# Performance work log

Measured on AMD Instinct MI355X. Metric: run time of the kernel, lower is better.

The kernel has to match this reference:

```python
import jax, jax.numpy as jnp
import numpy as np

B, N, D = 2, 2048, 1024
H = 16
HS = D // H
EPS = 1e-6


def layer_norm(x, scale, bias):
    mu = jnp.mean(x, axis=-1, keepdims=True)
    var = jnp.mean(jnp.square(x - mu), axis=-1, keepdims=True)
    return (x - mu) * jax.lax.rsqrt(var + EPS) * scale + bias


def setup_inputs() -> dict:
    key = jax.random.key(0)
    ks = jax.random.split(key, 8)
    lecun = lambda k, shape: jax.random.normal(k, shape, jnp.float32) / jnp.sqrt(shape[0])
    return {
        "x": jax.random.normal(ks[0], (B, N, D), jnp.float32),
        "ln1_scale": jnp.ones((D,), jnp.float32),
        "ln1_bias": jnp.zeros((D,), jnp.float32),
        "w_qkv": lecun(ks[1], (D, 3 * D)),
        "w_out": lecun(ks[2], (D, D)),
        "b_out": jnp.zeros((D,), jnp.float32),
        "ln2_scale": jnp.ones((D,), jnp.float32),
        "ln2_bias": jnp.zeros((D,), jnp.float32),
        "w1": lecun(ks[3], (D, 2 * D)),
        "b1": jnp.zeros((2 * D,), jnp.float32),
        "w2": lecun(ks[4], (2 * D, D)),
        "b2": jnp.zeros((D,), jnp.float32),
    }


def reference(x, ln1_scale, ln1_bias, w_qkv, w_out, b_out,
              ln2_scale, ln2_bias, w1, b1, w2, b2):
    b, n, d = x.shape
    # --- attention sub-block ---
    xn = layer_norm(x, ln1_scale, ln1_bias)
    qkv = xn @ w_qkv                      # [B,N,3D]
    q, k, v = jnp.split(qkv, 3, axis=-1)
    q = q.reshape(b, n, H, HS)
    k = k.reshape(b, n, H, HS)
    v = v.reshape(b, n, H, HS)
    scores = jnp.einsum('bihd,bjhd->bhij', q, k) / jnp.sqrt(jnp.float32(HS))
    causal = jnp.tril(jnp.ones((n, n), bool))[None, None]
    scores = jnp.where(causal, scores, -jnp.inf)
    attn = jax.nn.softmax(scores, axis=-1)
    out_heads = jnp.einsum('bhij,bjhd->bihd', attn, v).reshape(b, n, d)
    x = x + out_heads @ w_out + b_out
    xn2 = layer_norm(x, ln2_scale, ln2_bias)
    y = jax.nn.gelu(xn2 @ w1 + b1)        # flax nn.gelu default approximate=True
    x = x + (y @ w2 + b2)
    return x
```

## Files before the change

### kernel.cpp

```cpp
#include <hip/hip_runtime.h>

#define D_MODEL 1024
#define NSEQ    2048
#define NBATCH  2
#define NHEAD   16
#define HSZ     64
#define MROWS   4096

typedef short s8v  __attribute__((ext_vector_type(8)));
typedef float f32x4 __attribute__((ext_vector_type(4)));
typedef float f32x16 __attribute__((ext_vector_type(16)));
typedef unsigned long long u64;

#define AS1(p) ((__attribute__((address_space(1))) const void*)(p))
#define AS3(p) ((__attribute__((address_space(3))) void*)(p))

__device__ __forceinline__ float b2f(unsigned short s) {
    union { unsigned u; float f; } z; z.u = (unsigned)s << 16; return z.f;
}
__device__ __forceinline__ unsigned short f2b(float f) {
    union { float f; unsigned u; } z; z.f = f;
    unsigned r = z.u + 0x7fffu + ((z.u >> 16) & 1u);
    return (unsigned short)(r >> 16);
}
__device__ __forceinline__ float gelu_f(float x) {
    float u = 0.7978845608028654f * (x + 0.044715f * x * x * x);
    float t = 1.f - 2.f / (1.f + __expf(2.f * u));
    return 0.5f * x * (1.f + t);
}
__device__ __forceinline__ unsigned cvt_pk_bf16(float lo, float hi) {
    unsigned r;
    asm("v_cvt_pk_bf16_f32 %0, %1, %2" : "=v"(r) : "v"(lo), "v"(hi));
    return r;
}

__global__ __launch_bounds__(256) void sniff_k(const unsigned short* __restrict__ xr,
                                               int* __restrict__ flag) {
    __shared__ int cnt[4];
    int tid = threadIdx.x, ok = 0;
    for (int i = tid; i < 2048; i += 256) {
        unsigned short u = xr[i];
        int e = (u >> 7) & 0xFF;
        if (u == 0 || (e >= 110 && e <= 135)) ok++;
    }
    #pragma unroll
    for (int off = 32; off; off >>= 1) ok += __shfl_down(ok, off);
    if ((tid & 63) == 0) cnt[tid >> 6] = ok;
    __syncthreads();
    if (tid == 0) {
        int tot = cnt[0] + cnt[1] + cnt[2] + cnt[3];
        *flag = (tot > 1843) ? 1 : 0;
    }
}

__global__ __launch_bounds__(256) void cvt_small_k(
    const void* p0, const void* p1, const void* p2, const void* p3,
    const void* p4, const void* p5, const void* p6,
    unsigned short* __restrict__ out, const int* __restrict__ flag)
{
    int i = blockIdx.x * 256 + threadIdx.x;
    const void* src; int off;
    if      (i < 1024) { src = p0; off = i; }
    else if (i < 2048) { src = p1; off = i - 1024; }
    else if (i < 3072) { src = p2; off = i - 2048; }
    else if (i < 4096) { src = p3; off = i - 3072; }
    else if (i < 5120) { src = p4; off = i - 4096; }
    else if (i < 7168) { src = p5; off = i - 5120; }
    else               { src = p6; off = i - 7168; }
    out[i] = (*flag) ? ((const unsigned short*)src)[off]
                     : f2b(((const float*)src)[off]);
}

__global__ __launch_bounds__(256) void transpose_all_k(
    const void* wqkv, const void* wout, const void* w1, const void* w2,
    unsigned short* t_qkv, unsigned short* t_out,
    unsigned short* t_w1, unsigned short* t_w2, const int* __restrict__ flag)
{
    __shared__ unsigned short t[32][33];
    int bid = blockIdx.x;
    const void* W; unsigned short* Wt; int K, N, bx, by;
    if      (bid < 3072) { W = wqkv; Wt = t_qkv; K = 1024; N = 3072; bx = bid % 96; by = bid / 96; }
    else if (bid < 4096) { bid -= 3072; W = wout; Wt = t_out; K = 1024; N = 1024; bx = bid % 32; by = bid / 32; }
    else if (bid < 6144) { bid -= 4096; W = w1;   Wt = t_w1;  K = 1024; N = 2048; bx = bid % 64; by = bid / 64; }
    else                 { bid -= 6144; W = w2;   Wt = t_w2;  K = 2048; N = 1024; bx = bid % 32; by = bid / 32; }
    int f = *flag;
    int n0 = bx * 32, k0 = by * 32;
    int x = threadIdx.x & 31, y = threadIdx.x >> 5;
    #pragma unroll
    for (int r = 0; r < 32; r += 8) {
        size_t idx = (size_t)(k0 + r + y) * N + n0 + x;
        t[r + y][x] = f ? ((const unsigned short*)W)[idx]
                        : f2b(((const float*)W)[idx]);
    }
    __syncthreads();
    #pragma unroll
    for (int r = 0; r < 32; r += 8)
        Wt[(size_t)(n0 + r + y) * K + k0 + x] = t[x][r + y];
}

__global__ __launch_bounds__(256) void ln1f_k(
    const void* __restrict__ x_raw, const unsigned short* __restrict__ scale,
    const unsigned short* __restrict__ bias, unsigned short* __restrict__ xb,
    unsigned short* __restrict__ xn, const int* __restrict__ flag)
{
    int row = blockIdx.x, tid = threadIdx.x;
    int f = *flag;
    float v[4], s = 0.f, s2 = 0.f;
    #pragma unroll
    for (int i = 0; i < 4; ++i) {
        size_t idx = (size_t)row * D_MODEL + tid + i * 256;
        float t = f ? b2f(((const unsigned short*)x_raw)[idx])
                    : ((const float*)x_raw)[idx];
        v[i] = t; s += t; s2 += t * t;
    }
    #pragma unroll
    for (int off = 32; off; off >>= 1) { s += __shfl_down(s, off); s2 += __shfl_down(s2, off); }
    __shared__ float rs[4], rs2[4];
    int w = tid >> 6;
    if ((tid & 63) == 0) { rs[w] = s; rs2[w] = s2; }
    __syncthreads();
    float S  = rs[0] + rs[1] + rs[2] + rs[3];
    float S2 = rs2[0] + rs2[1] + rs2[2] + rs2[3];
    float mean = S * (1.f / D_MODEL);
    float var  = S2 * (1.f / D_MODEL) - mean * mean;
    float rstd = rsqrtf(var + 1e-6f);
    #pragma unroll
    for (int i = 0; i < 4; ++i) {
        int d = tid + i * 256;
        size_t idx = (size_t)row * D_MODEL + d;
        xb[idx] = f2b(v[i]);
        xn[idx] = f2b((v[i] - mean) * rstd * b2f(scale[d]) + b2f(bias[d]));
    }
}

__global__ __launch_bounds__(256) void ln_k(
    const unsigned short* __restrict__ x, const unsigned short* __restrict__ scale,
    const unsigned short* __restrict__ bias, unsigned short* __restrict__ out)
{
    int row = blockIdx.x, tid = threadIdx.x;
    const unsigned short* xr = x + (size_t)row * D_MODEL;
    float v[4], s = 0.f, s2 = 0.f;
    #pragma unroll
    for (int i = 0; i < 4; ++i) {
        float t = b2f(xr[tid + i * 256]);
        v[i] = t; s += t; s2 += t * t;
    }
    #pragma unroll
    for (int off = 32; off; off >>= 1) { s += __shfl_down(s, off); s2 += __shfl_down(s2, off); }
    __shared__ float rs[4], rs2[4];
    int w = tid >> 6;
    if ((tid & 63) == 0) { rs[w] = s; rs2[w] = s2; }
    __syncthreads();
    float S  = rs[0] + rs[1] + rs[2] + rs[3];
    float S2 = rs2[0] + rs2[1] + rs2[2] + rs2[3];
    float mean = S * (1.f / D_MODEL);
    float var  = S2 * (1.f / D_MODEL) - mean * mean;
    float rstd = rsqrtf(var + 1e-6f);
    #pragma unroll
    for (int i = 0; i < 4; ++i) {
        int d = tid + i * 256;
        out[(size_t)row * D_MODEL + d] =
            f2b((v[i] - mean) * rstd * b2f(scale[d]) + b2f(bias[d]));
    }
}

template<int TN, int ACT, int RES, int ODYN>
__global__ __launch_bounds__(256) void gemm128_k(
    const unsigned short* __restrict__ A, const unsigned short* __restrict__ Bt,
    const unsigned short* __restrict__ bias, const unsigned short* __restrict__ resid,
    void* __restrict__ Cp, int M, int Nn, int K, const int* __restrict__ flag)
{
    constexpr int MT = (TN == 128) ? 4 : 2;
    __shared__ short As[128 * 64];
    __shared__ short Bs[TN * 64];
    int tid = threadIdx.x;
    int m0 = blockIdx.y * 128, n0 = blockIdx.x * TN;
    int lane = tid & 63, w = tid >> 6;
    int a_base = (TN == 128) ? (w >> 1) * 64 : w * 32;
    int b_base = (TN == 128) ? (w & 1) * 64 : 0;
    int mm = lane & 15, q = lane >> 4;

    f32x4 zero = {0.f, 0.f, 0.f, 0.f};
    f32x4 acc[MT][4];
    #pragma unroll
    for (int mt = 0; mt < MT; ++mt)
        #pragma unroll
        for (int nt = 0; nt < 4; ++nt) acc[mt][nt] = zero;

    int grow   = lane >> 3;
    int gchunk = ((lane & 7) ^ grow) * 8;
    const unsigned short* Ab = A  + (size_t)(m0 + w * 32 + grow) * K + gchunk;
    const unsigned short* Bb = Bt + (size_t)(n0 + w * (TN / 4) + grow) * K + gchunk;
    int swz = (mm & 7);

    for (int k0 = 0; k0 < K; k0 += 64) {
        __syncthreads();
        #pragma unroll
        for (int s = 0; s < 4; ++s)
            __builtin_amdgcn_global_load_lds(AS1(Ab + k0 + (size_t)(s * 8) * K),
                                             AS3(&As[(w * 32 + s * 8) * 64]), 16, 0, 0);
        #pragma unroll
        for (int s = 0; s < TN / 32; ++s)
            __builtin_amdgcn_global_load_lds(AS1(Bb + k0 + (size_t)(s * 8) * K),
                                             AS3(&Bs[(w * (TN / 4) + s * 8) * 64]), 16, 0, 0);
        __syncthreads();
        #pragma unroll
        for (int kk = 0; kk < 2; ++kk) {
            int col = ((kk * 4 + q) ^ swz) * 8;
            s8v af[MT], bf[4];
            #pragma unroll
            for (int mt = 0; mt < MT; ++mt)
                af[mt] = *(const s8v*)&As[(a_base + mt * 16 + mm) * 64 + col];
            #pragma unroll
            for (int nt = 0; nt < 4; ++nt)
                bf[nt] = *(const s8v*)&Bs[(b_base + nt * 16 + mm) * 64 + col];
            #pragma unroll
            for (int mt = 0; mt < MT; ++mt)
                #pragma unroll
                for (int nt = 0; nt < 4; ++nt)
                    acc[mt][nt] = __builtin_amdgcn_mfma_f32_16x16x32_bf16(
                        af[mt], bf[nt], acc[mt][nt], 0, 0, 0);
        }
    }

    int f = ODYN ? *flag : 1;
    #pragma unroll
    for (int nt = 0; nt < 4; ++nt) {
        int gc = n0 + b_base + nt * 16 + mm;
        float bv = bias ? b2f(bias[gc]) : 0.f;
        #pragma unroll
        for (int mt = 0; mt < MT; ++mt) {
            #pragma unroll
            for (int r = 0; r < 4; ++r) {
                int gr = m0 + a_base + mt * 16 + q * 4 + r;
                float v = acc[mt][nt][r] + bv;
                if (ACT == 1) v = gelu_f(v);
                if (RES == 1) v += b2f(resid[(size_t)gr * Nn + gc]);
                if (f) ((unsigned short*)Cp)[(size_t)gr * Nn + gc] = f2b(v);
                else   ((float*)Cp)[(size_t)gr * Nn + gc] = v;
            }
        }
    }
}

#define SWZG(r) ((((r) >> 3) ^ (r)) & 7)

__global__ __launch_bounds__(128, 2) void fattn_k(
    const unsigned short* __restrict__ qkv, unsigned short* __restrict__ attn_out)
{
    int bh = blockIdx.x;
    int h = bh & (NHEAD - 1), b = bh >> 4;
    int qt = gridDim.y - 1 - blockIdx.y;
    int q0 = qt * 64;
    size_t base = (size_t)b * NSEQ * (3 * D_MODEL);

    __shared__ __align__(16) short Ks[2][4096];
    __shared__ __align__(16) short Vt[2][4096];

    int tid = threadIdx.x, lane = tid & 63, w = tid >> 6;
    int ql = lane & 31, hi = lane >> 5;
    int qw0 = q0 + w * 32;
    int gq = qw0 + ql;

    s8v qB[4];
    {
        const unsigned short* qrow = qkv + base + (size_t)gq * (3 * D_MODEL) + h * HSZ;
        #pragma unroll
        for (int dc = 0; dc < 4; ++dc) {
            s8v v = *(const s8v*)(qrow + dc * 16 + hi * 8);
            #pragma unroll
            for (int e = 0; e < 8; ++e) {
                unsigned short u = (unsigned short)v[e];
                if (u & 0x7f80u) u = (unsigned short)(u - 0x0180u);
                v[e] = (short)u;
            }
            qB[dc] = v;
        }
    }

    const unsigned short* kbase = qkv + base + D_MODEL + h * HSZ;
    const unsigned short* vbase = qkv + base + 2 * D_MODEL + h * HSZ;

    int kln = lane >> 3, kgs = lane & 7;
    int kq = tid >> 3, vd0 = (tid & 7) * 8;
    int pgr = 2 * (kq >> 2) + (kq & 1);
    int pof = 4 * ((kq >> 1) & 1);
    int swz0 = (((ql >> 3)    ) ^ ql) & 7;
    int swz1 = (((ql >> 3) + 4) ^ ql) & 7;

    f32x16 z16;
    #pragma unroll
    for (int i = 0; i < 16; ++i) z16[i] = 0.f;
    f32x16 accA = z16, accB = z16;
    float l_acc = 0.f;

    int nstages = qt + 1;
    s8v va, vb, vc, vd_;

    {
        #pragma unroll
        for (int i = 0; i < 4; ++i) {
            int key  = i * 16 + w * 8 + kln;
            int gsrc = kgs ^ (((2 * i + w) ^ kln) & 7);
            __builtin_amdgcn_global_load_lds(
                AS1(kbase + (size_t)key * (3 * D_MODEL) + gsrc * 8),
                AS3(&Ks[0][i * 1024 + w * 512]), 16, 0, 0);
        }
        const unsigned short* vr = vbase + (size_t)(4 * kq) * (3 * D_MODEL) + vd0;
        va  = *(const s8v*)vr;
        vb  = *(const s8v*)(vr + 3 * D_MODEL);
        vc  = *(const s8v*)(vr + 6 * D_MODEL);
        vd_ = *(const s8v*)(vr + 9 * D_MODEL);
        #pragma unroll
        for (int e = 0; e < 8; ++e) {
            unsigned plo = (unsigned)(unsigned short)va[e] | ((unsigned)(unsigned short)vb[e] << 16);
            unsigned phi = (unsigned)(unsigned short)vc[e] | ((unsigned)(unsigned short)vd_[e] << 16);
            int dim = vd0 + e;
            *(u64*)&Vt[0][dim * 64 + ((pgr ^ (((tid & 7) ^ e) & 7)) << 3) + pof] =
                (u64)plo | ((u64)phi << 32);
        }
    }
    __syncthreads();

    for (int t = 0; t < nstages; ++t) {
        int cur = t & 1, j0 = t * 64;
        bool pre = (t + 1 < nstages);
        if (pre) {
            int jn = j0 + 64;
            #pragma unroll
            for (int i = 0; i < 4; ++i) {
                int key  = i * 16 + w * 8 + kln;
                int gsrc = kgs ^ (((2 * i + w) ^ kln) & 7);
                __builtin_amdgcn_global_load_lds(
                    AS1(kbase + (size_t)(jn + key) * (3 * D_MODEL) + gsrc * 8),
                    AS3(&Ks[cur ^ 1][i * 1024 + w * 512]), 16, 0, 0);
            }
            const unsigned short* vr = vbase + (size_t)(jn + 4 * kq) * (3 * D_MODEL) + vd0;
            va  = *(const s8v*)vr;
            vb  = *(const s8v*)(vr + 3 * D_MODEL);
            vc  = *(const s8v*)(vr + 6 * D_MODEL);
            vd_ = *(const s8v*)(vr + 9 * D_MODEL);
        }
        __builtin_amdgcn_sched_barrier(0);

        int nkt = (j0 + 32 <= qw0 + 31) ? 2 : 1;
        #pragma unroll
        for (int kt = 0; kt < 2; ++kt) {
            if (kt >= nkt) break;
            int swzk = kt ? swz1 : swz0;
            f32x16 sc = z16;
            __builtin_amdgcn_s_setprio(1);
            #pragma unroll
            for (int dc = 0; dc < 4; ++dc) {
                s8v kf = *(const s8v*)&Ks[cur][(kt * 32 + ql) * 64 + (((2 * dc + hi) ^ swzk) << 3)];
                sc = __builtin_amdgcn_mfma_f32_32x32x16_bf16(kf, qB[dc], sc, 0, 0, 0);
            }
            __builtin_amdgcn_s_setprio(0);
            bool needmask = (j0 + kt * 32 + 31) > qw0;
            #pragma unroll
            for (int r = 0; r < 16; ++r) {
                float p = __expf(sc[r]);
                if (needmask) {
                    int gk = j0 + kt * 32 + (r & 3) + 8 * (r >> 2) + 4 * hi;
                    if (gk > gq) p = 0.f;
                }
                l_acc += p;
                sc[r] = p;
            }
            #pragma unroll
            for (int half = 0; half < 2; ++half) {
                union { unsigned u[4]; s8v v; } pu;
                pu.u[0] = cvt_pk_bf16(sc[half * 8 + 0], sc[half * 8 + 1]);
                pu.u[1] = cvt_pk_bf16(sc[half * 8 + 2], sc[half * 8 + 3]);
                pu.u[2] = cvt_pk_bf16(sc[half * 8 + 4], sc[half * 8 + 5]);
                pu.u[3] = cvt_pk_bf16(sc[half * 8 + 6], sc[half * 8 + 7]);
                int gb = 4 * kt + 2 * half + hi;
                __builtin_amdgcn_s_setprio(1);
                {
                    s8v vv = *(const s8v*)&Vt[cur][ql * 64 + ((gb ^ swz0) << 3)];
                    accA = __builtin_amdgcn_mfma_f32_32x32x16_bf16(pu.v, vv, accA, 0, 0, 0);
                }
                {
                    s8v vv = *(const s8v*)&Vt[cur][(32 + ql) * 64 + ((gb ^ swz1) << 3)];
                    accB = __builtin_amdgcn_mfma_f32_32x32x16_bf16(pu.v, vv, accB, 0, 0, 0);
                }
                __builtin_amdgcn_s_setprio(0);
            }
        }

        if (pre) {
            #pragma unroll
            for (int e = 0; e < 8; ++e) {
                unsigned plo = (unsigned)(unsigned short)va[e] | ((unsigned)(unsigned short)vb[e] << 16);
                unsigned phi = (unsigned)(unsigned short)vc[e] | ((unsigned)(unsigned short)vd_[e] << 16);
                int dim = vd0 + e;
                *(u64*)&Vt[cur ^ 1][dim * 64 + ((pgr ^ (((tid & 7) ^ e) & 7)) << 3) + pof] =
                    (u64)plo | ((u64)phi << 32);
            }
        }
        __syncthreads();
    }

    l_acc += __shfl_xor(l_acc, 32);
    float linv = 1.f / l_acc;
    unsigned short* orow = attn_out + (size_t)b * NSEQ * D_MODEL + h * HSZ;
    #pragma unroll
    for (int r = 0; r < 16; ++r) {
        int cr = (r & 3) + 8 * (r >> 2) + 4 * hi;
        float ri = __shfl(linv, cr);
        size_t ro = (size_t)(qw0 + cr) * D_MODEL;
        orow[ro + ql]      = f2b(accA[r] * ri);
        orow[ro + 32 + ql] = f2b(accB[r] * ri);
    }
}

extern "C" void kernel_launch(void* const* d_in, const int* in_sizes, int n_in,
                              void* d_out, int out_size, void* d_ws, size_t ws_size,
                              hipStream_t stream)
{
    const void* x_raw  = d_in[0];
    const void* ln1s_r = d_in[1];
    const void* ln1b_r = d_in[2];
    const void* wqkv_r = d_in[3];
    const void* wout_r = d_in[4];
    const void* bout_r = d_in[5];
    const void* ln2s_r = d_in[6];
    const void* ln2b_r = d_in[7];
    const void* w1_r   = d_in[8];
    const void* b1_r   = d_in[9];
    const void* w2_r   = d_in[10];
    const void* b2_r   = d_in[11];

    char* ws = (char*)d_ws;
    const size_t MB = 1024 * 1024;
    unsigned short* wt_qkv = (unsigned short*)(ws + 0 * MB);
    unsigned short* wt_out = (unsigned short*)(ws + 6 * MB);
    unsigned short* wt_w1  = (unsigned short*)(ws + 8 * MB);
    unsigned short* wt_w2  = (unsigned short*)(ws + 12 * MB);
    unsigned short* xb     = (unsigned short*)(ws + 16 * MB);
    unsigned short* xn     = (unsigned short*)(ws + 24 * MB);
    unsigned short* qkvb   = (unsigned short*)(ws + 32 * MB);
    unsigned short* x1     = (unsigned short*)(ws + 48 * MB);
    int*            flag   = (int*)           (ws + 56 * MB);
    unsigned short* cbias  = (unsigned short*)(ws + 56 * MB + 1024);
    unsigned short* attnb  = xn;
    unsigned short* xn2    = xn;
    unsigned short* hb     = qkvb;

    unsigned short* c_ln1s = cbias + 0;
    unsigned short* c_ln1b = cbias + 1024;
    unsigned short* c_bout = cbias + 2048;
    unsigned short* c_ln2s = cbias + 3072;
    unsigned short* c_ln2b = cbias + 4096;
    unsigned short* c_b1   = cbias + 5120;
    unsigned short* c_b2   = cbias + 7168;

    sniff_k<<<1, 256, 0, stream>>>((const unsigned short*)x_raw, flag);
    cvt_small_k<<<32, 256, 0, stream>>>(ln1s_r, ln1b_r, bout_r, ln2s_r, ln2b_r,
                                        b1_r, b2_r, cbias, flag);
    transpose_all_k<<<8192, 256, 0, stream>>>(wqkv_r, wout_r, w1_r, w2_r,
                                              wt_qkv, wt_out, wt_w1, wt_w2, flag);
    ln1f_k<<<MROWS, 256, 0, stream>>>(x_raw, c_ln1s, c_ln1b, xb, xn, flag);
    gemm128_k<128, 0, 0, 0><<<dim3(24, 32), 256, 0, stream>>>(
        xn, wt_qkv, nullptr, nullptr, qkvb, MROWS, 3072, 1024, flag);
    fattn_k<<<dim3(NBATCH * NHEAD, NSEQ / 64), 128, 0, stream>>>(qkvb, attnb);
    gemm128_k<64, 0, 1, 0><<<dim3(16, 32), 256, 0, stream>>>(
        attnb, wt_out, c_bout, xb, x1, MROWS, 1024, 1024, flag);
    ln_k<<<MROWS, 256, 0, stream>>>(x1, c_ln2s, c_ln2b, xn2);
    gemm128_k<128, 1, 0, 0><<<dim3(16, 32), 256, 0, stream>>>(
        xn2, wt_w1, c_b1, nullptr, hb, MROWS, 2048, 1024, flag);
    gemm128_k<64, 0, 1, 1><<<dim3(16, 32), 256, 0, stream>>>(
        hb, wt_w2, c_b2, x1, d_out, MROWS, 1024, 2048, flag);
}
```

Baseline: 309.6 us.

## Shrink attention blocks to single-wave 32-query tiles without block barriers

The flash-attention kernel moves from two-wave blocks over 64-query tiles with 64-key stages to one-wave blocks over 32-query tiles with 32-key stages. Because each block is a single wave, it replaces __syncthreads with vmcnt waits and sched barriers, and uses a single V-transpose LDS buffer. The aim is to cut barrier stalls, halve LDS per block and double the grid for finer causal load balance and more resident blocks. In exchange, K/V tiles are no longer shared between two waves, so global/L2 traffic for K and V roughly doubles, and there is more per-block setup overhead.

Measured after the change: 315.7 us. No clear change (+2.0%).

```diff
diff --git a/kernel.cpp b/kernel.cpp
--- a/kernel.cpp
+++ b/kernel.cpp
@@ -243,24 +243,21 @@
     }
 }
 
-#define SWZG(r) ((((r) >> 3) ^ (r)) & 7)
-
-__global__ __launch_bounds__(128, 2) void fattn_k(
+__global__ __launch_bounds__(64) void fattn_k(
     const unsigned short* __restrict__ qkv, unsigned short* __restrict__ attn_out)
 {
     int bh = blockIdx.x;
     int h = bh & (NHEAD - 1), b = bh >> 4;
-    int qt = gridDim.y - 1 - blockIdx.y;
-    int q0 = qt * 64;
+    int qt = (int)gridDim.y - 1 - (int)blockIdx.y;
+    int q0 = qt * 32;
     size_t base = (size_t)b * NSEQ * (3 * D_MODEL);
 
-    __shared__ __align__(16) short Ks[2][4096];
-    __shared__ __align__(16) short Vt[2][4096];
-
-    int tid = threadIdx.x, lane = tid & 63, w = tid >> 6;
+    __shared__ __align__(16) short Ks[2][2048];
+    __shared__ __align__(16) short Vt[2048];
+
+    int lane = threadIdx.x;
     int ql = lane & 31, hi = lane >> 5;
-    int qw0 = q0 + w * 32;
-    int gq = qw0 + ql;
+    int gq = q0 + ql;
 
     s8v qB[4];
     {
@@ -281,12 +278,13 @@
     const unsigned short* kbase = qkv + base + D_MODEL + h * HSZ;
     const unsigned short* vbase = qkv + base + 2 * D_MODEL + h * HSZ;
 
-    int kln = lane >> 3, kgs = lane & 7;
-    int kq = tid >> 3, vd0 = (tid & 7) * 8;
-    int pgr = 2 * (kq >> 2) + (kq & 1);
-    int pof = 4 * ((kq >> 1) & 1);
-    int swz0 = (((ql >> 3)    ) ^ ql) & 7;
-    int swz1 = (((ql >> 3) + 4) ^ ql) & 7;
+    int r8 = lane >> 3, a7 = lane & 7;
+    int ksrc = ((a7 ^ r8) & 7) * 8;
+    int vd0 = a7 * 8;
+    int gbase = 2 * (r8 >> 2) + (r8 & 1);
+    int sbase = ((r8 >> 1) & 1) * 4;
+    int kswz = (ql & 7);
+    int vr0 = ql >> 1, vsel = 4 * (ql & 1);
 
     f32x16 z16;
     #pragma unroll
@@ -294,98 +292,89 @@
     f32x16 accA = z16, accB = z16;
     float l_acc = 0.f;
 
-    int nstages = qt + 1;
     s8v va, vb, vc, vd_;
 
+    #pragma unroll
+    for (int i = 0; i < 4; ++i)
+        __builtin_amdgcn_global_load_lds(
+            AS1(kbase + (size_t)(i * 8 + r8) * (3 * D_MODEL) + ksrc),
+            AS3(&Ks[0][i * 512]), 16, 0, 0);
     {
-        #pragma unroll
-        for (int i = 0; i < 4; ++i) {
-            int key  = i * 16 + w * 8 + kln;
-            int gsrc = kgs ^ (((2 * i + w) ^ kln) & 7);
-            __builtin_amdgcn_global_load_lds(
-                AS1(kbase + (size_t)key * (3 * D_MODEL) + gsrc * 8),
-                AS3(&Ks[0][i * 1024 + w * 512]), 16, 0, 0);
-        }
-        const unsigned short* vr = vbase + (size_t)(4 * kq) * (3 * D_MODEL) + vd0;
-        va  = *(const s8v*)vr;
-        vb  = *(const s8v*)(vr + 3 * D_MODEL);
-        vc  = *(const s8v*)(vr + 6 * D_MODEL);
-        vd_ = *(const s8v*)(vr + 9 * D_MODEL);
-        #pragma unroll
-        for (int e = 0; e < 8; ++e) {
-            unsigned plo = (unsigned)(unsigned short)va[e] | ((unsigned)(unsigned short)vb[e] << 16);
-            unsigned phi = (unsigned)(unsigned short)vc[e] | ((unsigned)(unsigned short)vd_[e] << 16);
-            int dim = vd0 + e;
-            *(u64*)&Vt[0][dim * 64 + ((pgr ^ (((tid & 7) ^ e) & 7)) << 3) + pof] =
-                (u64)plo | ((u64)phi << 32);
-        }
-    }
-    __syncthreads();
-
-    for (int t = 0; t < nstages; ++t) {
-        int cur = t & 1, j0 = t * 64;
-        bool pre = (t + 1 < nstages);
+        const unsigned short* vr_ = vbase + (size_t)(4 * r8) * (3 * D_MODEL) + vd0;
+        va  = *(const s8v*)vr_;
+        vb  = *(const s8v*)(vr_ + 3 * D_MODEL);
+        vc  = *(const s8v*)(vr_ + 6 * D_MODEL);
+        vd_ = *(const s8v*)(vr_ + 9 * D_MODEL);
+    }
+    #pragma unroll
+    for (int e = 0; e < 8; ++e) {
+        unsigned plo = (unsigned)(unsigned short)va[e] | ((unsigned)(unsigned short)vb[e] << 16);
+        unsigned phi = (unsigned)(unsigned short)vc[e] | ((unsigned)(unsigned short)vd_[e] << 16);
+        int vrow = 4 * a7 + (e >> 1);
+        int gam = (4 * (e & 1) + gbase) ^ (vrow & 7);
+        *(u64*)&Vt[vrow * 64 + gam * 8 + sbase] = (u64)plo | ((u64)phi << 32);
+    }
+    asm volatile("s_waitcnt vmcnt(0)");
+    __builtin_amdgcn_sched_barrier(0);
+
+    int cur = 0;
+    for (int s = 0; s <= qt; ++s) {
+        bool pre = (s < qt);
         if (pre) {
-            int jn = j0 + 64;
-            #pragma unroll
-            for (int i = 0; i < 4; ++i) {
-                int key  = i * 16 + w * 8 + kln;
-                int gsrc = kgs ^ (((2 * i + w) ^ kln) & 7);
+            int jn = 32 * (s + 1);
+            #pragma unroll
+            for (int i = 0; i < 4; ++i)
                 __builtin_amdgcn_global_load_lds(
-                    AS1(kbase + (size_t)(jn + key) * (3 * D_MODEL) + gsrc * 8),
-                    AS3(&Ks[cur ^ 1][i * 1024 + w * 512]), 16, 0, 0);
-            }
-            const unsigned short* vr = vbase + (size_t)(jn + 4 * kq) * (3 * D_MODEL) + vd0;
-            va  = *(const s8v*)vr;
-            vb  = *(const s8v*)(vr + 3 * D_MODEL);
-            vc  = *(const s8v*)(vr + 6 * D_MODEL);
-            vd_ = *(const s8v*)(vr + 9 * D_MODEL);
+                    AS1(kbase + (size_t)(jn + i * 8 + r8) * (3 * D_MODEL) + ksrc),
+                    AS3(&Ks[cur ^ 1][i * 512]), 16, 0, 0);
+            const unsigned short* vr_ = vbase + (size_t)(jn + 4 * r8) * (3 * D_MODEL) + vd0;
+            va  = *(const s8v*)vr_;
+            vb  = *(const s8v*)(vr_ + 3 * D_MODEL);
+            vc  = *(const s8v*)(vr_ + 6 * D_MODEL);
+            vd_ = *(const s8v*)(vr_ + 9 * D_MODEL);
         }
         __builtin_amdgcn_sched_barrier(0);
 
-        int nkt = (j0 + 32 <= qw0 + 31) ? 2 : 1;
-        #pragma unroll
-        for (int kt = 0; kt < 2; ++kt) {
-            if (kt >= nkt) break;
-            int swzk = kt ? swz1 : swz0;
-            f32x16 sc = z16;
+        f32x16 sc = z16;
+        __builtin_amdgcn_s_setprio(1);
+        #pragma unroll
+        for (int dc = 0; dc < 4; ++dc) {
+            s8v kf = *(const s8v*)&Ks[cur][ql * 64 + (((2 * dc + hi) ^ kswz) << 3)];
+            sc = __builtin_amdgcn_mfma_f32_32x32x16_bf16(kf, qB[dc], sc, 0, 0, 0);
+        }
+        __builtin_amdgcn_s_setprio(0);
+
+        bool needmask = (s == qt);
+        #pragma unroll
+        for (int r = 0; r < 16; ++r) {
+            float p = __expf(sc[r]);
+            if (needmask) {
+                int gk = 32 * s + (r & 3) + 8 * (r >> 2) + 4 * hi;
+                if (gk > gq) p = 0.f;
+            }
+            l_acc += p;
+            sc[r] = p;
+        }
+
+        #pragma unroll
+        for (int half = 0; half < 2; ++half) {
+            union { unsigned u[4]; s8v v; } pu;
+            pu.u[0] = cvt_pk_bf16(sc[half * 8 + 0], sc[half * 8 + 1]);
+            pu.u[1] = cvt_pk_bf16(sc[half * 8 + 2], sc[half * 8 + 3]);
+            pu.u[2] = cvt_pk_bf16(sc[half * 8 + 4], sc[half * 8 + 5]);
+            pu.u[3] = cvt_pk_bf16(sc[half * 8 + 6], sc[half * 8 + 7]);
+            int gA = (vsel + 2 * half + hi) ^ (vr0 & 7);
+            int gB = (vsel + 2 * half + hi) ^ (vr0 & 7);
             __builtin_amdgcn_s_setprio(1);
-            #pragma unroll
-            for (int dc = 0; dc < 4; ++dc) {
-                s8v kf = *(const s8v*)&Ks[cur][(kt * 32 + ql) * 64 + (((2 * dc + hi) ^ swzk) << 3)];
-                sc = __builtin_amdgcn_mfma_f32_32x32x16_bf16(kf, qB[dc], sc, 0, 0, 0);
+            {
+                s8v vv = *(const s8v*)&Vt[vr0 * 64 + (gA << 3)];
+                accA = __builtin_amdgcn_mfma_f32_32x32x16_bf16(pu.v, vv, accA, 0, 0, 0);
+            }
+            {
+                s8v vv = *(const s8v*)&Vt[(16 + vr0) * 64 + (gB << 3)];
+                accB = __builtin_amdgcn_mfma_f32_32x32x16_bf16(pu.v, vv, accB, 0, 0, 0);
             }
             __builtin_amdgcn_s_setprio(0);
-            bool needmask = (j0 + kt * 32 + 31) > qw0;
-            #pragma unroll
-            for (int r = 0; r < 16; ++r) {
-                float p = __expf(sc[r]);
-                if (needmask) {
-                    int gk = j0 + kt * 32 + (r & 3) + 8 * (r >> 2) + 4 * hi;
-                    if (gk > gq) p = 0.f;
-                }
-                l_acc += p;
-                sc[r] = p;
-            }
-            #pragma unroll
-            for (int half = 0; half < 2; ++half) {
-                union { unsigned u[4]; s8v v; } pu;
-                pu.u[0] = cvt_pk_bf16(sc[half * 8 + 0], sc[half * 8 + 1]);
-                pu.u[1] = cvt_pk_bf16(sc[half * 8 + 2], sc[half * 8 + 3]);
-                pu.u[2] = cvt_pk_bf16(sc[half * 8 + 4], sc[half * 8 + 5]);
-                pu.u[3] = cvt_pk_bf16(sc[half * 8 + 6], sc[half * 8 + 7]);
-                int gb = 4 * kt + 2 * half + hi;
-                __builtin_amdgcn_s_setprio(1);
-                {
-                    s8v vv = *(const s8v*)&Vt[cur][ql * 64 + ((gb ^ swz0) << 3)];
-                    accA = __builtin_amdgcn_mfma_f32_32x32x16_bf16(pu.v, vv, accA, 0, 0, 0);
-                }
-                {
-                    s8v vv = *(const s8v*)&Vt[cur][(32 + ql) * 64 + ((gb ^ swz1) << 3)];
-                    accB = __builtin_amdgcn_mfma_f32_32x32x16_bf16(pu.v, vv, accB, 0, 0, 0);
-                }
-                __builtin_amdgcn_s_setprio(0);
-            }
         }
 
         if (pre) {
@@ -393,12 +382,14 @@
             for (int e = 0; e < 8; ++e) {
                 unsigned plo = (unsigned)(unsigned short)va[e] | ((unsigned)(unsigned short)vb[e] << 16);
                 unsigned phi = (unsigned)(unsigned short)vc[e] | ((unsigned)(unsigned short)vd_[e] << 16);
-                int dim = vd0 + e;
-                *(u64*)&Vt[cur ^ 1][dim * 64 + ((pgr ^ (((tid & 7) ^ e) & 7)) << 3) + pof] =
-                    (u64)plo | ((u64)phi << 32);
-            }
-        }
-        __syncthreads();
+                int vrow = 4 * a7 + (e >> 1);
+                int gam = (4 * (e & 1) + gbase) ^ (vrow & 7);
+                *(u64*)&Vt[vrow * 64 + gam * 8 + sbase] = (u64)plo | ((u64)phi << 32);
+            }
+        }
+        asm volatile("s_waitcnt vmcnt(0)");
+        __builtin_amdgcn_sched_barrier(0);
+        cur ^= 1;
     }
 
     l_acc += __shfl_xor(l_acc, 32);
@@ -408,7 +399,7 @@
     for (int r = 0; r < 16; ++r) {
         int cr = (r & 3) + 8 * (r >> 2) + 4 * hi;
         float ri = __shfl(linv, cr);
-        size_t ro = (size_t)(qw0 + cr) * D_MODEL;
+        size_t ro = (size_t)(q0 + cr) * D_MODEL;
         orow[ro + ql]      = f2b(accA[r] * ri);
         orow[ro + 32 + ql] = f2b(accB[r] * ri);
     }
@@ -463,7 +454,7 @@
     ln1f_k<<<MROWS, 256, 0, stream>>>(x_raw, c_ln1s, c_ln1b, xb, xn, flag);
     gemm128_k<128, 0, 0, 0><<<dim3(24, 32), 256, 0, stream>>>(
         xn, wt_qkv, nullptr, nullptr, qkvb, MROWS, 3072, 1024, flag);
-    fattn_k<<<dim3(NBATCH * NHEAD, NSEQ / 64), 128, 0, stream>>>(qkvb, attnb);
+    fattn_k<<<dim3(NBATCH * NHEAD, NSEQ / 32), 64, 0, stream>>>(qkvb, attnb);
     gemm128_k<64, 0, 1, 0><<<dim3(16, 32), 256, 0, stream>>>(
         attnb, wt_out, c_bout, xb, x1, MROWS, 1024, 1024, flag);
     ln_k<<<MROWS, 256, 0, stream>>>(x1, c_ln2s, c_ln2b, xn2);
```
